# Performance work log

Hardware: AMD Instinct MI355X
Metric: run time of the kernel (lower is better)

The kernel has to match this reference:

```python
import jax, jax.numpy as jnp
import numpy as np

DIM = 1024
N_HEADS = 16
HEAD_DIM = DIM // N_HEADS  # 64
B, T = 2, 2048


def setup_inputs() -> dict:
    key = jax.random.key(0)
    k1, k2, k3, k4, k5 = jax.random.split(key, 5)
    x = jax.random.normal(k1, (B, T, DIM), dtype=jnp.float32)
    cos = jax.random.uniform(k2, (1, 1, T, HEAD_DIM // 2), dtype=jnp.float32)
    sin = jax.random.uniform(k3, (1, 1, T, HEAD_DIM // 2), dtype=jnp.float32)
    # torch Linear weights: y = x @ W.T ; qkv: [3*dim, dim], out_proj: [dim, dim]
    w_qkv = jax.random.normal(k4, (3 * DIM, DIM), dtype=jnp.float32) * 0.02
    w_out = jax.random.normal(k5, (DIM, DIM), dtype=jnp.float32) * 0.02
    return {"x": x, "cos": cos, "sin": sin, "w_qkv": w_qkv, "w_out": w_out}


def _rope(t, cos, sin):
    # t: [B, H, T, D]; cos/sin broadcast as [1,1,T,D/2]
    t1, t2 = jnp.split(t, 2, axis=-1)
    return jnp.concatenate([t1 * cos - t2 * sin, t1 * sin + t2 * cos], axis=-1)


def reference(x, cos, sin, w_qkv, w_out):
    Bb, Tt, C = x.shape
    qkv = x @ w_qkv.T                                    # [B, T, 3C]
    q, k, v = jnp.split(qkv, 3, axis=-1)
    def heads(t):
        return t.reshape(Bb, Tt, N_HEADS, HEAD_DIM).transpose(0, 2, 1, 3)
    q, k, v = heads(q), heads(k), heads(v)               # [B, H, T, D]
    q = _rope(q, cos, sin)
    k = _rope(k, cos, sin)
    scale = 1.0 / jnp.sqrt(jnp.float32(HEAD_DIM))
    scores = jnp.einsum("bhqd,bhkd->bhqk", q, k) * scale  # [B, H, T, T]
    causal = jnp.tril(jnp.ones((Tt, Tt), dtype=bool))
    scores = jnp.where(causal[None, None], scores, jnp.float32(-jnp.inf))
    attn = jax.nn.softmax(scores, axis=-1)
    out = jnp.einsum("bhqk,bhkd->bhqd", attn, v)          # [B, H, T, D]
    out = out.transpose(0, 2, 1, 3).reshape(Bb, Tt, C)
    return out @ w_out.T
```

## Files before the change

kernel.cpp:

```cpp
#include <hip/hip_runtime.h>

#define DIMC 1024
#define NH   16
#define HD   64
#define BSZ  2
#define TSZ  2048
#define MROWS (BSZ*TSZ)

typedef __attribute__((ext_vector_type(8))) short s16x8;
typedef __attribute__((ext_vector_type(4))) float f32x4;

__device__ __forceinline__ float b2f(unsigned short u) {
  return __uint_as_float(((unsigned)u) << 16);
}
__device__ __forceinline__ unsigned short f2b(float f) {
  unsigned x = __float_as_uint(f);
  unsigned r = x + 0x7fffu + ((x >> 16) & 1u);
  return (unsigned short)(r >> 16);
}
__device__ __forceinline__ unsigned pk2(float a, float b) {
  unsigned r;
  asm("v_cvt_pk_bf16_f32 %0, %1, %2" : "=v"(r) : "v"(a), "v"(b));
  return r;
}
__device__ __forceinline__ float ex2(float x) {
#if __has_builtin(__builtin_amdgcn_exp2f)
  return __builtin_amdgcn_exp2f(x);
#else
  float r; asm("v_exp_f32 %0, %1" : "=v"(r) : "v"(x)); return r;
#endif
}
__device__ __forceinline__ float ldsc(const void* __restrict__ p, int idx, int isf32) {
  return isf32 ? ((const float*)p)[idx] : b2f(((const unsigned short*)p)[idx]);
}

__device__ __forceinline__ void async_cp16(const unsigned short* g, unsigned short* l) {
  __builtin_amdgcn_global_load_lds(
      (const __attribute__((address_space(1))) unsigned int*)g,
      (__attribute__((address_space(3))) unsigned int*)l, 16, 0, 0);
}

__global__ void detect_dtype(const unsigned short* __restrict__ cosp, int* __restrict__ flag) {
  const int i = threadIdx.x;
  const unsigned long long m = __ballot(cosp[i] >= 0x4000u);
  if (i == 0) *flag = (m != 0ull) ? 1 : 0;
}

__global__ __launch_bounds__(256)
void cvt_all(const float* __restrict__ x, const float* __restrict__ wq,
             const float* __restrict__ wo,
             unsigned short* __restrict__ xb, unsigned short* __restrict__ wqb,
             unsigned short* __restrict__ wob, const int* __restrict__ flag) {
  if (*flag == 0) return;
  const unsigned id = blockIdx.x * 256 + threadIdx.x;
  const float* src; unsigned short* dst; unsigned off;
  if (id < 524288u) { src = x; dst = xb; off = id; }
  else if (id < 917504u) { src = wq; dst = wqb; off = id - 524288u; }
  else { src = wo; dst = wob; off = id - 917504u; }
  const float4 a = ((const float4*)src)[off * 2];
  const float4 b = ((const float4*)src)[off * 2 + 1];
  uint4 u;
  u.x = pk2(a.x, a.y); u.y = pk2(a.z, a.w);
  u.z = pk2(b.x, b.y); u.w = pk2(b.z, b.w);
  ((uint4*)dst)[off] = u;
}

__global__ __launch_bounds__(512, 4)
void gemm_qkv128(const void* __restrict__ Aorig, const unsigned short* __restrict__ Aconv,
                 const void* __restrict__ Worig, const unsigned short* __restrict__ Wconv,
                 const void* __restrict__ cosp, const void* __restrict__ sinp,
                 unsigned short* __restrict__ qout,
                 unsigned short* __restrict__ kout,
                 unsigned short* __restrict__ vout,
                 const int* __restrict__ dflag) {
  const int f32flag = *dflag;
  const unsigned short* A = f32flag ? Aconv : (const unsigned short*)Aorig;
  const unsigned short* W = f32flag ? Wconv : (const unsigned short*)Worig;

  const int tid = threadIdx.x;
  const int m0 = blockIdx.y * 128;
  const int n0 = blockIdx.x * 128;

  __shared__ __align__(16) unsigned short s_ab[2 * 128 * 64];
  unsigned short* s_a = s_ab;
  unsigned short* s_b = s_ab + 128 * 64;

  const int lane = tid & 63;
  const int wave = tid >> 6;
  const int wm = (wave & 3) * 32;
  const int wn = (wave >> 2) * 64;
  const int m16 = lane & 15;
  const int quad = lane >> 4;

  const int srow = lane >> 3;
  const int schunk = (lane & 7) ^ srow;

  f32x4 acc[2][4];
#pragma unroll
  for (int i = 0; i < 2; ++i)
#pragma unroll
    for (int j = 0; j < 4; ++j) acc[i][j] = (f32x4){0.f, 0.f, 0.f, 0.f};

  for (int kt = 0; kt < DIMC; kt += 64) {
    __syncthreads();
#pragma unroll
    for (int u = 0; u < 2; ++u) {
      const int r0 = u * 64 + wave * 8;
      async_cp16(A + (size_t)(m0 + r0 + srow) * DIMC + kt + schunk * 8, &s_a[r0 * 64]);
      async_cp16(W + (size_t)(n0 + r0 + srow) * DIMC + kt + schunk * 8, &s_b[r0 * 64]);
    }
    __syncthreads();
#pragma unroll
    for (int kk = 0; kk < 64; kk += 32) {
      const int cx = ((kk >> 3) + quad) ^ (m16 & 7);
      s16x8 af[2], bf[4];
#pragma unroll
      for (int i = 0; i < 2; ++i)
        af[i] = *(const s16x8*)&s_a[(wm + i * 16 + m16) * 64 + cx * 8];
#pragma unroll
      for (int j = 0; j < 4; ++j)
        bf[j] = *(const s16x8*)&s_b[(wn + j * 16 + m16) * 64 + cx * 8];
#pragma unroll
      for (int i = 0; i < 2; ++i)
#pragma unroll
        for (int j = 0; j < 4; ++j)
          acc[i][j] = __builtin_amdgcn_mfma_f32_16x16x32_bf16(af[i], bf[j], acc[i][j], 0, 0, 0);
    }
  }

  const int sel = n0 >> 10;
  const int h = ((n0 & 1023) >> 6) + (wave >> 2);
  unsigned short* dst = (sel == 0) ? qout : ((sel == 1) ? kout : vout);
  const float qsc = (sel == 0) ? 0.18033688f : 1.0f;
  __syncthreads();
  unsigned short* tile = s_ab + wave * 2048;
  if (sel < 2) {
#pragma unroll
    for (int i = 0; i < 2; ++i)
#pragma unroll
      for (int r = 0; r < 4; ++r) {
        const int row_l = i * 16 + quad * 4 + r;
        const int t = (m0 + wm + row_l) & 2047;
#pragma unroll
        for (int jg = 0; jg < 2; ++jg) {
          const int d = jg * 16 + m16;
          const float c = ldsc(cosp, t * 32 + d, f32flag);
          const float sn = ldsc(sinp, t * 32 + d, f32flag);
          const float v1 = acc[i][jg][r];
          const float v2 = acc[i][jg + 2][r];
          tile[row_l * 64 + d]      = f2b((v1 * c - v2 * sn) * qsc);
          tile[row_l * 64 + d + 32] = f2b((v1 * sn + v2 * c) * qsc);
        }
      }
  } else {
#pragma unroll
    for (int i = 0; i < 2; ++i)
#pragma unroll
      for (int r = 0; r < 4; ++r) {
        const int row_l = i * 16 + quad * 4 + r;
#pragma unroll
        for (int j = 0; j < 4; ++j)
          tile[row_l * 64 + j * 16 + m16] = f2b(acc[i][j][r]);
      }
  }
#pragma unroll
  for (int s = 0; s < 4; ++s) {
    const int row_l = s * 8 + (lane >> 3);
    const int seg = lane & 7;
    const int mrow_ = m0 + wm + row_l;
    const int bb = mrow_ >> 11;
    const int t = mrow_ & 2047;
    unsigned short* drow = dst + (((size_t)(bb * NH + h)) * TSZ + t) * HD;
    *(uint4*)(drow + seg * 8) = *(const uint4*)&tile[row_l * 64 + seg * 8];
  }
}

template <int EPI>
__global__ __launch_bounds__(256)
void gemm_bt_async(const void* __restrict__ Aorig, const unsigned short* __restrict__ Aconv,
                   const void* __restrict__ Worig, const unsigned short* __restrict__ Wconv,
                   void* __restrict__ C,
                   const int* __restrict__ dflag, int Nsz) {
  const int f32flag = *dflag;
  const unsigned short* A = f32flag ? Aconv : (const unsigned short*)Aorig;
  const unsigned short* W = f32flag ? Wconv : (const unsigned short*)Worig;

  const int tid = threadIdx.x;
  const int m0 = blockIdx.y * 128;
  const int n0 = blockIdx.x * 64;

  __shared__ __align__(16) unsigned short s_ab[128 * 64 + 64 * 64];
  unsigned short* s_a = s_ab;
  unsigned short* s_b = s_ab + 128 * 64;

  const int lane = tid & 63;
  const int wave = tid >> 6;
  const int wm = wave * 32;
  const int m16 = lane & 15;
  const int quad = lane >> 4;

  const int srow = lane >> 3;
  const int schunk = (lane & 7) ^ srow;

  f32x4 acc[2][4];
#pragma unroll
  for (int i = 0; i < 2; ++i)
#pragma unroll
    for (int j = 0; j < 4; ++j) acc[i][j] = (f32x4){0.f, 0.f, 0.f, 0.f};

  for (int kt = 0; kt < DIMC; kt += 64) {
    __syncthreads();
#pragma unroll
    for (int u = 0; u < 4; ++u) {
      const int r0 = u * 32 + wave * 8;
      async_cp16(A + (size_t)(m0 + r0 + srow) * DIMC + kt + schunk * 8, &s_a[r0 * 64]);
    }
#pragma unroll
    for (int u = 0; u < 2; ++u) {
      const int r0 = u * 32 + wave * 8;
      async_cp16(W + (size_t)(n0 + r0 + srow) * DIMC + kt + schunk * 8, &s_b[r0 * 64]);
    }
    __syncthreads();
#pragma unroll
    for (int kk = 0; kk < 64; kk += 32) {
      const int cx = ((kk >> 3) + quad) ^ (m16 & 7);
      s16x8 af[2], bf[4];
#pragma unroll
      for (int i = 0; i < 2; ++i)
        af[i] = *(const s16x8*)&s_a[(wm + i * 16 + m16) * 64 + cx * 8];
#pragma unroll
      for (int j = 0; j < 4; ++j)
        bf[j] = *(const s16x8*)&s_b[(j * 16 + m16) * 64 + cx * 8];
#pragma unroll
      for (int i = 0; i < 2; ++i)
#pragma unroll
        for (int j = 0; j < 4; ++j)
          acc[i][j] = __builtin_amdgcn_mfma_f32_16x16x32_bf16(af[i], bf[j], acc[i][j], 0, 0, 0);
    }
  }

  if (f32flag) {
    float* Cf = (float*)C;
#pragma unroll
    for (int i = 0; i < 2; ++i)
#pragma unroll
      for (int j = 0; j < 4; ++j)
#pragma unroll
        for (int r = 0; r < 4; ++r) {
          const int mrow_ = m0 + wm + i * 16 + quad * 4 + r;
          const int col = n0 + j * 16 + m16;
          Cf[(size_t)mrow_ * Nsz + col] = acc[i][j][r];
        }
  } else {
    unsigned short* Ch = (unsigned short*)C;
#pragma unroll
    for (int i = 0; i < 2; ++i)
#pragma unroll
      for (int j = 0; j < 4; ++j)
#pragma unroll
        for (int r = 0; r < 4; ++r) {
          const int mrow_ = m0 + wm + i * 16 + quad * 4 + r;
          const int col = n0 + j * 16 + m16;
          Ch[(size_t)mrow_ * Nsz + col] = f2b(acc[i][j][r]);
        }
  }
}

__device__ __forceinline__ void attn_pass(
    const unsigned short* __restrict__ qgh, const unsigned short* __restrict__ kgh,
    const unsigned short* __restrict__ vgh, unsigned short* __restrict__ outg,
    int b, int h, int qs, int nc, unsigned short* s_k0, unsigned short* s_k1,
    unsigned short* s_v0, unsigned short* s_v1, unsigned short* s_p,
    int tid, int lane, int w, int m16, int quad) {
  const unsigned short* qrow = qgh + (size_t)(qs + m16) * HD;
  const s16x8 bq0 = *(const s16x8*)(qrow + quad * 8);
  const s16x8 bq1 = *(const s16x8*)(qrow + 32 + quad * 8);

  f32x4 oacc[4];
#pragma unroll
  for (int dt = 0; dt < 4; ++dt) oacc[dt] = (f32x4){0.f, 0.f, 0.f, 0.f};
  float m_ = -1e30f, l_ = 0.f;

  const int krow = tid >> 3, kseg = tid & 7;
  const int vkey = tid & 63, vseg = tid >> 6;

  {
    const uint4 pk = *(const uint4*)(kgh + (size_t)krow * HD + kseg * 8);
    const uint4 pv = *(const uint4*)(vgh + (size_t)vkey * HD + vseg * 8);
    *(uint4*)&s_k0[krow * 72 + kseg * 8] = pk;
    const unsigned short* vv = (const unsigned short*)&pv;
#pragma unroll
    for (int jj = 0; jj < 8; ++jj) s_v0[(vseg * 8 + jj) * 72 + vkey] = vv[jj];
  }

  for (int kc = 0; kc < nc; ++kc) {
    unsigned short* sk = (kc & 1) ? s_k1 : s_k0;
    unsigned short* sv = (kc & 1) ? s_v1 : s_v0;
    unsigned short* skN = (kc & 1) ? s_k0 : s_k1;
    unsigned short* svN = (kc & 1) ? s_v0 : s_v1;
    __syncthreads();
    uint4 pk, pv;
    const int pf = (kc + 1 < nc);
    if (pf) {
      pk = *(const uint4*)(kgh + (size_t)((kc + 1) * 64 + krow) * HD + kseg * 8);
      pv = *(const uint4*)(vgh + (size_t)((kc + 1) * 64 + vkey) * HD + vseg * 8);
    }

    if (kc * 64 <= qs + 15) {
      f32x4 sacc[4];
#pragma unroll
      for (int jt = 0; jt < 4; ++jt) sacc[jt] = (f32x4){0.f, 0.f, 0.f, 0.f};
      __builtin_amdgcn_s_setprio(1);
#pragma unroll
      for (int jt = 0; jt < 4; ++jt) {
        const s16x8 ak0 = *(const s16x8*)&sk[(jt * 16 + m16) * 72 + quad * 8];
        sacc[jt] = __builtin_amdgcn_mfma_f32_16x16x32_bf16(ak0, bq0, sacc[jt], 0, 0, 0);
        const s16x8 ak1 = *(const s16x8*)&sk[(jt * 16 + m16) * 72 + 32 + quad * 8];
        sacc[jt] = __builtin_amdgcn_mfma_f32_16x16x32_bf16(ak1, bq1, sacc[jt], 0, 0, 0);
      }
      __builtin_amdgcn_s_setprio(0);

      if (kc * 64 + 63 > qs) {
#pragma unroll
        for (int jt = 0; jt < 4; ++jt)
#pragma unroll
          for (int r = 0; r < 4; ++r)
            if (kc * 64 + jt * 16 + quad * 4 + r > qs + m16) sacc[jt][r] = -1e30f;
      }

      float mx = sacc[0][0];
#pragma unroll
      for (int jt = 0; jt < 4; ++jt)
#pragma unroll
        for (int r = 0; r < 4; ++r) mx = fmaxf(mx, sacc[jt][r]);
      mx = fmaxf(mx, __shfl_xor(mx, 16, 64));
      mx = fmaxf(mx, __shfl_xor(mx, 32, 64));
      if (!__all(mx <= m_ + 8.0f)) {
        const float mn = fmaxf(m_, mx);
        const float alpha = ex2(m_ - mn);
        m_ = mn;
        l_ *= alpha;
#pragma unroll
        for (int dt = 0; dt < 4; ++dt)
#pragma unroll
          for (int r = 0; r < 4; ++r) oacc[dt][r] *= alpha;
      }
      float rs = 0.f;
#pragma unroll
      for (int jt = 0; jt < 4; ++jt)
#pragma unroll
        for (int r = 0; r < 4; ++r) {
          const float p = ex2(sacc[jt][r] - m_);
          sacc[jt][r] = p;
          rs += p;
        }
      rs += __shfl_xor(rs, 16, 64);
      rs += __shfl_xor(rs, 32, 64);
      l_ += rs;

#pragma unroll
      for (int jt = 0; jt < 4; ++jt) {
        uint2 pw;
        pw.x = pk2(sacc[jt][0], sacc[jt][1]);
        pw.y = pk2(sacc[jt][2], sacc[jt][3]);
        *(uint2*)&s_p[(w * 16 + m16) * 72 + jt * 16 + quad * 4] = pw;
      }

      __builtin_amdgcn_s_setprio(1);
#pragma unroll
      for (int kk = 0; kk < 64; kk += 32) {
        const s16x8 bp = *(const s16x8*)&s_p[(w * 16 + m16) * 72 + kk + quad * 8];
#pragma unroll
        for (int dt = 0; dt < 4; ++dt) {
          const s16x8 av = *(const s16x8*)&sv[(dt * 16 + m16) * 72 + kk + quad * 8];
          oacc[dt] = __builtin_amdgcn_mfma_f32_16x16x32_bf16(av, bp, oacc[dt], 0, 0, 0);
        }
      }
      __builtin_amdgcn_s_setprio(0);
    }

    if (pf) {
      *(uint4*)&skN[krow * 72 + kseg * 8] = pk;
      const unsigned short* vv = (const unsigned short*)&pv;
#pragma unroll
      for (int jj = 0; jj < 8; ++jj) svN[(vseg * 8 + jj) * 72 + vkey] = vv[jj];
    }
  }

  const float linv = 1.0f / l_;
#pragma unroll
  for (int dt = 0; dt < 4; ++dt) {
    uint2 ow;
    ow.x = pk2(oacc[dt][0] * linv, oacc[dt][1] * linv);
    ow.y = pk2(oacc[dt][2] * linv, oacc[dt][3] * linv);
    *(uint2*)&s_p[(w * 16 + m16) * 72 + dt * 16 + quad * 4] = ow;
  }
  {
    const int qq = lane >> 2, dseg = lane & 3;
    const uint4 o0 = *(const uint4*)&s_p[(w * 16 + qq) * 72 + dseg * 16];
    const uint4 o1 = *(const uint4*)&s_p[(w * 16 + qq) * 72 + dseg * 16 + 8];
    unsigned short* orow =
        outg + ((size_t)b * TSZ + qs + qq) * DIMC + h * 64 + dseg * 16;
    *(uint4*)orow = o0;
    *(uint4*)(orow + 8) = o1;
  }
}

__global__ __launch_bounds__(512)
void attn_fwd_mfma(const unsigned short* __restrict__ qg,
                   const unsigned short* __restrict__ kg,
                   const unsigned short* __restrict__ vg,
                   unsigned short* __restrict__ outg) {
  const int tid = threadIdx.x;
  const int lane = tid & 63;
  const int w = tid >> 6;
  const int m16 = lane & 15;
  const int quad = lane >> 4;
  const int l = (int)blockIdx.x;
  const int g = (l & 255) >> 5;
  const int p = (l < 256) ? g : (15 - g);
  const int nc = 32 - p;
  const int bh = l & 31;
  const int b = bh >> 4, h = bh & 15;
  const size_t base = (size_t)bh * TSZ * HD;
  const int sub = (w < 4) ? p : (31 - p);
  const int qs = sub * 64 + (w & 3) * 16;

  __shared__ __align__(16) unsigned short s_k0[64 * 72];
  __shared__ __align__(16) unsigned short s_k1[64 * 72];
  __shared__ __align__(16) unsigned short s_v0[64 * 72];
  __shared__ __align__(16) unsigned short s_v1[64 * 72];
  __shared__ __align__(16) unsigned short s_p[128 * 72];

  attn_pass(qg + base, kg + base, vg + base, outg, b, h, qs, nc,
            s_k0, s_k1, s_v0, s_v1, s_p, tid, lane, w, m16, quad);
}

extern "C" void kernel_launch(void* const* d_in, const int* in_sizes, int n_in,
                              void* d_out, int out_size, void* d_ws, size_t ws_size,
                              hipStream_t stream) {
  (void)in_sizes; (void)n_in; (void)out_size; (void)ws_size;
  const void* x    = d_in[0];
  const void* cosp = d_in[1];
  const void* sinp = d_in[2];
  const void* wqkv = d_in[3];
  const void* wout = d_in[4];

  int* dflag = (int*)d_ws;
  const size_t per = (size_t)BSZ * NH * TSZ * HD;
  unsigned short* q = (unsigned short*)((char*)d_ws + 256);
  unsigned short* k = q + per;
  unsigned short* v = k + per;
  unsigned short* attnb = v + per;
  unsigned short* xb   = attnb + (size_t)MROWS * DIMC;
  unsigned short* wqb  = xb + (size_t)MROWS * DIMC;
  unsigned short* wob  = wqb + (size_t)3 * DIMC * DIMC;

  detect_dtype<<<1, 64, 0, stream>>>((const unsigned short*)cosp, dflag);
  cvt_all<<<dim3(4096), dim3(256), 0, stream>>>(
      (const float*)x, (const float*)wqkv, (const float*)wout, xb, wqb, wob, dflag);
  gemm_qkv128<<<dim3(3 * DIMC / 128, MROWS / 128), dim3(512), 0, stream>>>(
      x, xb, wqkv, wqb, cosp, sinp, q, k, v, dflag);
  attn_fwd_mfma<<<dim3(512), dim3(512), 0, stream>>>(q, k, v, attnb);
  gemm_bt_async<0><<<dim3(DIMC / 64, MROWS / 128), dim3(256), 0, stream>>>(
      attnb, attnb, wout, wob, d_out, dflag, DIMC);
}
```

Before: 183.0 us.

## Double-buffer LDS tiles in QKV and output GEMMs, stage fp32 output via LDS

Both GEMM kernels now use two LDS buffers, issuing the async copy of the next K-slice before computing on the current one. This removes one barrier per iteration and lets global loads overlap MFMA work. MFMA sections are wrapped in s_setprio to favour compute waves. The output GEMM's fp32 epilogue now goes through a padded LDS tile so global stores are coalesced float4 writes. The cost is double the LDS footprint, which may lower occupancy for the 512-thread QKV kernel.

New measurement: 177.7 us. -2.9%, faster.

```diff
diff --git a/kernel.cpp b/kernel.cpp
--- a/kernel.cpp
+++ b/kernel.cpp
@@ -81,9 +81,7 @@
   const int m0 = blockIdx.y * 128;
   const int n0 = blockIdx.x * 128;
 
-  __shared__ __align__(16) unsigned short s_ab[2 * 128 * 64];
-  unsigned short* s_a = s_ab;
-  unsigned short* s_b = s_ab + 128 * 64;
+  __shared__ __align__(16) unsigned short s_ab[2 * 16384];
 
   const int lane = tid & 63;
   const int wave = tid >> 6;
@@ -95,44 +93,57 @@
   const int srow = lane >> 3;
   const int schunk = (lane & 7) ^ srow;
 
+  const unsigned short* ga = A + (size_t)(m0 + wave * 8 + srow) * DIMC + schunk * 8;
+  const unsigned short* gb = W + (size_t)(n0 + wave * 8 + srow) * DIMC + schunk * 8;
+
   f32x4 acc[2][4];
 #pragma unroll
   for (int i = 0; i < 2; ++i)
 #pragma unroll
     for (int j = 0; j < 4; ++j) acc[i][j] = (f32x4){0.f, 0.f, 0.f, 0.f};
 
-  for (int kt = 0; kt < DIMC; kt += 64) {
-    __syncthreads();
+  auto stage = [&](int b, int kt) {
+    unsigned short* sa = s_ab + b * 16384;
 #pragma unroll
     for (int u = 0; u < 2; ++u) {
-      const int r0 = u * 64 + wave * 8;
-      async_cp16(A + (size_t)(m0 + r0 + srow) * DIMC + kt + schunk * 8, &s_a[r0 * 64]);
-      async_cp16(W + (size_t)(n0 + r0 + srow) * DIMC + kt + schunk * 8, &s_b[r0 * 64]);
-    }
-    __syncthreads();
+      async_cp16(ga + (size_t)(u * 64) * DIMC + kt, &sa[(u * 64 + wave * 8) * 64]);
+      async_cp16(gb + (size_t)(u * 64) * DIMC + kt, &sa[8192 + (u * 64 + wave * 8) * 64]);
+    }
+  };
+
+  stage(0, 0);
+  __syncthreads();
+
+  for (int t = 0; t < 16; ++t) {
+    const int cur = t & 1;
+    if (t < 15) stage(cur ^ 1, (t + 1) * 64);
+    const unsigned short* sa = s_ab + cur * 16384;
+    const unsigned short* sb = sa + 8192;
+    __builtin_amdgcn_s_setprio(1);
 #pragma unroll
     for (int kk = 0; kk < 64; kk += 32) {
       const int cx = ((kk >> 3) + quad) ^ (m16 & 7);
       s16x8 af[2], bf[4];
 #pragma unroll
       for (int i = 0; i < 2; ++i)
-        af[i] = *(const s16x8*)&s_a[(wm + i * 16 + m16) * 64 + cx * 8];
+        af[i] = *(const s16x8*)&sa[(wm + i * 16 + m16) * 64 + cx * 8];
 #pragma unroll
       for (int j = 0; j < 4; ++j)
-        bf[j] = *(const s16x8*)&s_b[(wn + j * 16 + m16) * 64 + cx * 8];
+        bf[j] = *(const s16x8*)&sb[(wn + j * 16 + m16) * 64 + cx * 8];
 #pragma unroll
       for (int i = 0; i < 2; ++i)
 #pragma unroll
         for (int j = 0; j < 4; ++j)
           acc[i][j] = __builtin_amdgcn_mfma_f32_16x16x32_bf16(af[i], bf[j], acc[i][j], 0, 0, 0);
     }
+    __builtin_amdgcn_s_setprio(0);
+    __syncthreads();
   }
 
   const int sel = n0 >> 10;
   const int h = ((n0 & 1023) >> 6) + (wave >> 2);
   unsigned short* dst = (sel == 0) ? qout : ((sel == 1) ? kout : vout);
   const float qsc = (sel == 0) ? 0.18033688f : 1.0f;
-  __syncthreads();
   unsigned short* tile = s_ab + wave * 2048;
   if (sel < 2) {
 #pragma unroll
@@ -175,12 +186,10 @@
   }
 }
 
-template <int EPI>
 __global__ __launch_bounds__(256)
-void gemm_bt_async(const void* __restrict__ Aorig, const unsigned short* __restrict__ Aconv,
-                   const void* __restrict__ Worig, const unsigned short* __restrict__ Wconv,
-                   void* __restrict__ C,
-                   const int* __restrict__ dflag, int Nsz) {
+void gemm_out(const void* __restrict__ Aorig, const unsigned short* __restrict__ Aconv,
+              const void* __restrict__ Worig, const unsigned short* __restrict__ Wconv,
+              void* __restrict__ C, const int* __restrict__ dflag, int Nsz) {
   const int f32flag = *dflag;
   const unsigned short* A = f32flag ? Aconv : (const unsigned short*)Aorig;
   const unsigned short* W = f32flag ? Wconv : (const unsigned short*)Worig;
@@ -189,9 +198,7 @@
   const int m0 = blockIdx.y * 128;
   const int n0 = blockIdx.x * 64;
 
-  __shared__ __align__(16) unsigned short s_ab[128 * 64 + 64 * 64];
-  unsigned short* s_a = s_ab;
-  unsigned short* s_b = s_ab + 128 * 64;
+  __shared__ __align__(16) unsigned short s_ab[2 * 12288];
 
   const int lane = tid & 63;
   const int wave = tid >> 6;
@@ -202,55 +209,72 @@
   const int srow = lane >> 3;
   const int schunk = (lane & 7) ^ srow;
 
+  const unsigned short* ga = A + (size_t)(m0 + wave * 8 + srow) * DIMC + schunk * 8;
+  const unsigned short* gb = W + (size_t)(n0 + wave * 8 + srow) * DIMC + schunk * 8;
+
   f32x4 acc[2][4];
 #pragma unroll
   for (int i = 0; i < 2; ++i)
 #pragma unroll
     for (int j = 0; j < 4; ++j) acc[i][j] = (f32x4){0.f, 0.f, 0.f, 0.f};
 
-  for (int kt = 0; kt < DIMC; kt += 64) {
-    __syncthreads();
-#pragma unroll
-    for (int u = 0; u < 4; ++u) {
-      const int r0 = u * 32 + wave * 8;
-      async_cp16(A + (size_t)(m0 + r0 + srow) * DIMC + kt + schunk * 8, &s_a[r0 * 64]);
-    }
-#pragma unroll
-    for (int u = 0; u < 2; ++u) {
-      const int r0 = u * 32 + wave * 8;
-      async_cp16(W + (size_t)(n0 + r0 + srow) * DIMC + kt + schunk * 8, &s_b[r0 * 64]);
-    }
-    __syncthreads();
+  auto stage = [&](int b, int kt) {
+    unsigned short* sa = s_ab + b * 12288;
+#pragma unroll
+    for (int u = 0; u < 4; ++u)
+      async_cp16(ga + (size_t)(u * 32) * DIMC + kt, &sa[(u * 32 + wave * 8) * 64]);
+#pragma unroll
+    for (int u = 0; u < 2; ++u)
+      async_cp16(gb + (size_t)(u * 32) * DIMC + kt, &sa[8192 + (u * 32 + wave * 8) * 64]);
+  };
+
+  stage(0, 0);
+  __syncthreads();
+
+  for (int t = 0; t < 16; ++t) {
+    const int cur = t & 1;
+    if (t < 15) stage(cur ^ 1, (t + 1) * 64);
+    const unsigned short* sa = s_ab + cur * 12288;
+    const unsigned short* sb = sa + 8192;
+    __builtin_amdgcn_s_setprio(1);
 #pragma unroll
     for (int kk = 0; kk < 64; kk += 32) {
       const int cx = ((kk >> 3) + quad) ^ (m16 & 7);
       s16x8 af[2], bf[4];
 #pragma unroll
       for (int i = 0; i < 2; ++i)
-        af[i] = *(const s16x8*)&s_a[(wm + i * 16 + m16) * 64 + cx * 8];
+        af[i] = *(const s16x8*)&sa[(wm + i * 16 + m16) * 64 + cx * 8];
 #pragma unroll
       for (int j = 0; j < 4; ++j)
-        bf[j] = *(const s16x8*)&s_b[(j * 16 + m16) * 64 + cx * 8];
+        bf[j] = *(const s16x8*)&sb[(j * 16 + m16) * 64 + cx * 8];
 #pragma unroll
       for (int i = 0; i < 2; ++i)
 #pragma unroll
         for (int j = 0; j < 4; ++j)
           acc[i][j] = __builtin_amdgcn_mfma_f32_16x16x32_bf16(af[i], bf[j], acc[i][j], 0, 0, 0);
     }
+    __builtin_amdgcn_s_setprio(0);
+    __syncthreads();
   }
 
   if (f32flag) {
+    float* ftile = (float*)s_ab + wave * (32 * 68);
+#pragma unroll
+    for (int i = 0; i < 2; ++i)
+#pragma unroll
+      for (int j = 0; j < 4; ++j)
+#pragma unroll
+        for (int r = 0; r < 4; ++r)
+          ftile[(i * 16 + quad * 4 + r) * 68 + j * 16 + m16] = acc[i][j][r];
     float* Cf = (float*)C;
 #pragma unroll
     for (int i = 0; i < 2; ++i)
 #pragma unroll
-      for (int j = 0; j < 4; ++j)
-#pragma unroll
-        for (int r = 0; r < 4; ++r) {
-          const int mrow_ = m0 + wm + i * 16 + quad * 4 + r;
-          const int col = n0 + j * 16 + m16;
-          Cf[(size_t)mrow_ * Nsz + col] = acc[i][j][r];
-        }
+      for (int s = 0; s < 4; ++s) {
+        const int row_l = i * 16 + s * 4 + (lane >> 4);
+        const float4 vv = *(const float4*)&ftile[row_l * 68 + (lane & 15) * 4];
+        *(float4*)&Cf[(size_t)(m0 + wm + row_l) * Nsz + n0 + (lane & 15) * 4] = vv;
+      }
   } else {
     unsigned short* Ch = (unsigned short*)C;
 #pragma unroll
@@ -462,6 +486,6 @@
   gemm_qkv128<<<dim3(3 * DIMC / 128, MROWS / 128), dim3(512), 0, stream>>>(
       x, xb, wqkv, wqb, cosp, sinp, q, k, v, dflag);
   attn_fwd_mfma<<<dim3(512), dim3(512), 0, stream>>>(q, k, v, attnb);
-  gemm_bt_async<0><<<dim3(DIMC / 64, MROWS / 128), dim3(256), 0, stream>>>(
+  gemm_out<<<dim3(DIMC / 64, MROWS / 128), dim3(256), 0, stream>>>(
       attnb, attnb, wout, wob, d_out, dflag, DIMC);
 }
```
